# Performance work log

Hardware: AMD Instinct MI355X
Metric: run time of the kernel (lower is better)

## Reference

```python
import jax, jax.numpy as jnp
import numpy as np

HID = 512
HEADS = 8
HEAD_DIM = HID // HEADS
BS, SEQ = 4, 2048


def setup_inputs() -> dict:
    key = jax.random.key(0)
    ks = jax.random.split(key, 12)
    s = 0.02
    return {
        "query": jax.random.normal(ks[0], (BS, SEQ, HID), jnp.float32),
        "key": jax.random.normal(ks[1], (BS, SEQ, HID), jnp.float32),
        "value": jax.random.normal(ks[2], (BS, SEQ, HID), jnp.float32),
        "query_mask": jnp.ones((BS, SEQ), dtype=bool),
        "key_mask": jnp.ones((BS, SEQ), dtype=bool),
        "Wq": jax.random.normal(ks[3], (HID, HID), jnp.float32) * s,
        "bq": jnp.zeros((HID,), jnp.float32),
        "Wk": jax.random.normal(ks[4], (HID, HID), jnp.float32) * s,
        "bk": jnp.zeros((HID,), jnp.float32),
        "Wv": jax.random.normal(ks[5], (HID, HID), jnp.float32) * s,
        "bv": jnp.zeros((HID,), jnp.float32),
        "Wo": jax.random.normal(ks[6], (HID, HID), jnp.float32) * s,
        "bo": jnp.zeros((HID,), jnp.float32),
    }


def _mha(query, key, value, query_mask, key_mask, Wq, bq, Wk, bk, Wv, bv, Wo, bo):
    bs, q_len, _ = query.shape
    k_len = key.shape[1]
    scale = jnp.sqrt(jnp.asarray(HEAD_DIM, query.dtype))

    def proj(x, W, b):  # nn.Linear: x @ W^T + b, then split heads -> [b,h,s,d]
        y = jnp.einsum('bse,fe->bsf', x, W) + b
        return y.reshape(bs, -1, HEADS, HEAD_DIM).transpose(0, 2, 1, 3)

    q = proj(query, Wq, bq)
    k = proj(key, Wk, bk)
    v = proj(value, Wv, bv)

    energy = jnp.einsum('bhqd,bhkd->bhqk', q, k) / scale  # [b,h,q,k]
    neg = -jnp.finfo(energy.dtype).max

    pad_mask = query_mask[:, None, :, None] & key_mask[:, None, None, :]
    energy = jnp.where(pad_mask, energy, neg)

    # causal: mask positions where q_idx < k_idx
    causal = jnp.arange(q_len)[:, None] < jnp.arange(k_len)[None, :]
    energy = jnp.where(causal[None, None], neg, energy)

    attn = jax.nn.softmax(energy, axis=-1)  # dropout p=0.0 -> identity
    x = jnp.einsum('bhqk,bhkd->bhqd', attn, v)
    x = x.transpose(0, 2, 1, 3).reshape(bs, q_len, HID)
    return jnp.einsum('bse,fe->bsf', x, Wo) + bo


def reference(query, key, value, query_mask, key_mask, Wq, bq, Wk, bk, Wv, bv, Wo, bo):
    return _mha(query, key, value, query_mask, key_mask, Wq, bq, Wk, bk, Wv, bv, Wo, bo)
```

## Files before the change

### kernel.cpp

```cpp
#include <hip/hip_runtime.h>
#include <hip/hip_bf16.h>

#define DEVI __device__ __forceinline__

typedef __attribute__((ext_vector_type(4)))  float f32x4;
typedef __attribute__((ext_vector_type(16))) float f32x16;
typedef __attribute__((ext_vector_type(8)))  short bf16x8;

constexpr int BS    = 4;
constexpr int SEQ   = 2048;
constexpr int HID   = 512;
constexpr int HEADS = 8;
constexpr int HD    = 64;
constexpr int M     = BS * SEQ;

constexpr float QSCALE = 0.125f * 1.4426950408889634f;

DEVI ushort f2bf(float f) {
    union { float f; unsigned u; } a; a.f = f;
    unsigned r = a.u + 0x7fffu + ((a.u >> 16) & 1u);
    return (ushort)(r >> 16);
}

DEVI f32x4 mfma16(bf16x8 a, bf16x8 b, f32x4 c) {
    return __builtin_amdgcn_mfma_f32_16x16x32_bf16(a, b, c, 0, 0, 0);
}
DEVI f32x16 mfma32(bf16x8 a, bf16x8 b, f32x16 c) {
    return __builtin_amdgcn_mfma_f32_32x32x16_bf16(a, b, c, 0, 0, 0);
}

DEVI void gl_lds16(const ushort* g, ushort* l) {
    __builtin_amdgcn_global_load_lds(
        (const __attribute__((address_space(1))) void*)g,
        (__attribute__((address_space(3))) void*)l,
        16, 0, 0);
}

DEVI unsigned cvtpk(float lo, float hi) {
    unsigned r;
    asm("v_cvt_pk_bf16_f32 %0, %1, %2" : "=v"(r) : "v"(lo), "v"(hi));
    return r;
}

__global__ void cast_w(const float* __restrict__ wq, const float* __restrict__ wk,
                       const float* __restrict__ wv, const float* __restrict__ wo,
                       ushort* __restrict__ oq, ushort* __restrict__ ok,
                       ushort* __restrict__ ov, ushort* __restrict__ oo)
{
    const int NW4 = HID * HID / 4;
    int i = blockIdx.x * blockDim.x + threadIdx.x;
    const int a = i >> 16, j = i & (NW4 - 1);
    const float* src = (a == 0) ? wq : (a == 1) ? wk : (a == 2) ? wv : wo;
    ushort* dst = (a == 0) ? oq : (a == 1) ? ok : (a == 2) ? ov : oo;
    float4 f = ((const float4*)src)[j];
    ushort4 u;
    u.x = f2bf(f.x); u.y = f2bf(f.y); u.z = f2bf(f.z); u.w = f2bf(f.w);
    ((ushort4*)dst)[j] = u;
}

template<bool AF32>
DEVI void gemm_core(const void* __restrict__ Ain, const ushort* __restrict__ W,
                    const float* __restrict__ bias, void* __restrict__ out,
                    float scale, int mode, ushort* lA, ushort* lB)
{
    constexpr int BK = 32;
    const int tid  = threadIdx.x;
    const int lane = tid & 63, w = tid >> 6;
    const int wm = w >> 1, wn = w & 1;
    const int l15 = lane & 15, lg = lane >> 4;
    const int m0 = blockIdx.x * 128, n0 = blockIdx.y * 128;
    const int srow = tid >> 2, sc8 = (tid & 3) * 8;
    const int arow = tid >> 1, ach = (tid & 1) * 16;

    f32x4 acc[4][4];
    #pragma unroll
    for (int i = 0; i < 4; i++)
        #pragma unroll
        for (int n = 0; n < 4; n++) acc[i][n] = f32x4{0.f, 0.f, 0.f, 0.f};

    for (int k0 = 0; k0 < HID; k0 += BK) {
        if constexpr (AF32) {
            const float4* ap = (const float4*)((const float*)Ain +
                                (size_t)(m0 + arow) * HID + k0 + ach);
            const float4 a0 = ap[0], a1 = ap[1], a2 = ap[2], a3 = ap[3];
            union { unsigned u[4]; bf16x8 v; } p0, p1;
            p0.u[0] = cvtpk(a0.x, a0.y); p0.u[1] = cvtpk(a0.z, a0.w);
            p0.u[2] = cvtpk(a1.x, a1.y); p0.u[3] = cvtpk(a1.z, a1.w);
            p1.u[0] = cvtpk(a2.x, a2.y); p1.u[1] = cvtpk(a2.z, a2.w);
            p1.u[2] = cvtpk(a3.x, a3.y); p1.u[3] = cvtpk(a3.z, a3.w);
            *(bf16x8*)(lA + arow * 32 + ach)     = p0.v;
            *(bf16x8*)(lA + arow * 32 + ach + 8) = p1.v;
        } else {
            const ushort* A = (const ushort*)Ain;
            gl_lds16(A + (size_t)(m0 + srow) * HID + k0 + sc8, lA + w * 512);
            gl_lds16(A + (size_t)(m0 + 64 + srow) * HID + k0 + sc8, lA + 2048 + w * 512);
        }
        gl_lds16(W + (size_t)(n0 + srow) * HID + k0 + sc8, lB + w * 512);
        gl_lds16(W + (size_t)(n0 + 64 + srow) * HID + k0 + sc8, lB + 2048 + w * 512);
        __syncthreads();

        bf16x8 af[4], bfr[4];
        #pragma unroll
        for (int i = 0; i < 4; i++)
            af[i] = *(const bf16x8*)(lA + (wm * 64 + i * 16 + l15) * BK + lg * 8);
        #pragma unroll
        for (int n = 0; n < 4; n++)
            bfr[n] = *(const bf16x8*)(lB + (wn * 64 + n * 16 + l15) * BK + lg * 8);
        #pragma unroll
        for (int i = 0; i < 4; i++)
            #pragma unroll
            for (int n = 0; n < 4; n++)
                acc[i][n] = mfma16(af[i], bfr[n], acc[i][n]);
        __syncthreads();
    }

    #pragma unroll
    for (int i = 0; i < 4; i++) {
        #pragma unroll
        for (int n = 0; n < 4; n++) {
            const int col = n0 + wn * 64 + n * 16 + l15;
            const float bb = bias[col];
            const int rbase = m0 + wm * 64 + i * 16 + lg * 4;
            #pragma unroll
            for (int jj = 0; jj < 4; jj++) {
                float v = (acc[i][n][jj] + bb) * scale;
                const int r = rbase + jj;
                if (mode == 3) {
                    ((float*)out)[(size_t)r * HID + col] = v;
                } else {
                    const int b = r >> 11, s = r & (SEQ - 1);
                    const int h = col >> 6, d = col & 63;
                    const int bh = b * HEADS + h;
                    const int t = s >> 5;
                    const ushort u = f2bf(v);
                    if (mode == 0) {
                        const int l31r = s & 31;
                        const int ds = d >> 4, hif = (d >> 3) & 1, jf = d & 7;
                        ((ushort*)out)[(((size_t)bh * 64 + t) * 4 + ds) * 512 +
                                       (hif * 32 + l31r) * 8 + jf] = u;
                    } else {
                        const int c = s & 31;
                        const int kvh = (c >> 4) & 1, hif = (c >> 2) & 1;
                        const int jf = (c & 3) + ((c >> 3) & 1) * 4;
                        const int dt = d >> 5, drow = d & 31;
                        ((ushort*)out)[(((size_t)bh * 64 + t) * 4 + dt * 2 + kvh) * 512 +
                                       (hif * 32 + drow) * 8 + jf] = u;
                    }
                }
            }
        }
    }
}

__global__ __launch_bounds__(256)
void gemm_qkv(const float* __restrict__ Xq, const float* __restrict__ Xk,
              const float* __restrict__ Xv,
              const ushort* __restrict__ Wq, const ushort* __restrict__ Wk,
              const ushort* __restrict__ Wv,
              const float* __restrict__ bq, const float* __restrict__ bk,
              const float* __restrict__ bv,
              ushort* __restrict__ Qf, ushort* __restrict__ Kf,
              ushort* __restrict__ Vf)
{
    __shared__ ushort lA[128 * 32];
    __shared__ ushort lB[128 * 32];
    const int z = blockIdx.z;
    const float* A = z == 0 ? Xq : z == 1 ? Xk : Xv;
    const ushort* W = z == 0 ? Wq : z == 1 ? Wk : Wv;
    const float* bias = z == 0 ? bq : z == 1 ? bk : bv;
    void* out = z == 0 ? (void*)Qf : z == 1 ? (void*)Kf : (void*)Vf;
    gemm_core<true>(A, W, bias, out, z == 0 ? QSCALE : 1.0f, z == 2 ? 2 : 0, lA, lB);
}

__global__ __launch_bounds__(256)
void gemm_o(const ushort* __restrict__ ctx, const ushort* __restrict__ Wo,
            const float* __restrict__ bo, float* __restrict__ out)
{
    __shared__ ushort lA[128 * 32];
    __shared__ ushort lB[128 * 32];
    gemm_core<false>(ctx, Wo, bo, out, 1.0f, 3, lA, lB);
}

__global__ __launch_bounds__(256)
void attn5(const ushort* __restrict__ Qf, const ushort* __restrict__ Kf,
           const ushort* __restrict__ Vf, ushort* __restrict__ ctx)
{
    __shared__ float part[4][2][16][64];
    __shared__ float pml[4][2][32];

    const int tid  = threadIdx.x;
    const int lane = tid & 63, w = tid >> 6;
    const int l31 = lane & 31, hi = lane >> 5;

    const int bid = blockIdx.x;
    const int bh  = bid & 31;
    const int qt  = 63 - (bid >> 5);
    const int qb  = qt * 32;

    const ushort* Qb = Qf + ((size_t)bh * 64 + qt) * 2048;
    const ushort* Kb = Kf + (size_t)bh * 64 * 2048;
    const ushort* Vb = Vf + (size_t)bh * 64 * 2048;

    bf16x8 qf[4];
    #pragma unroll
    for (int ds = 0; ds < 4; ds++)
        qf[ds] = *(const bf16x8*)(Qb + ds * 512 + lane * 8);

    f32x16 acc0 = {}, acc1 = {};
    float mrun = -3e38f, lrun = 0.f;

    bf16x8 kf[4] = {}, va[4] = {};
    if (w <= qt) {
        const ushort* kp = Kb + (size_t)w * 2048 + lane * 8;
        const ushort* vp = Vb + (size_t)w * 2048 + lane * 8;
        #pragma unroll
        for (int ds = 0; ds < 4; ds++) {
            kf[ds] = *(const bf16x8*)(kp + ds * 512);
            va[ds] = *(const bf16x8*)(vp + ds * 512);
        }
    }

    for (int t = w; t <= qt; t += 4) {
        f32x16 s = {};
        #pragma unroll
        for (int ds = 0; ds < 4; ds++)
            s = mfma32(kf[ds], qf[ds], s);

        bf16x8 kfn[4], van[4];
        {
            const int tn = (t + 4 <= qt) ? t + 4 : t;
            const ushort* kp = Kb + (size_t)tn * 2048 + lane * 8;
            const ushort* vp = Vb + (size_t)tn * 2048 + lane * 8;
            #pragma unroll
            for (int ds = 0; ds < 4; ds++) {
                kfn[ds] = *(const bf16x8*)(kp + ds * 512);
                van[ds] = *(const bf16x8*)(vp + ds * 512);
            }
        }

        if (t == qt) {
            #pragma unroll
            for (int r = 0; r < 16; r++) {
                const int kvrow = (r & 3) + 8 * (r >> 2) + 4 * hi;
                s[r] = (kvrow > l31) ? -3e38f : s[r];
            }
        }

        float m8[8];
        #pragma unroll
        for (int r = 0; r < 8; r++) m8[r] = fmaxf(s[r], s[r + 8]);
        float m4a = fmaxf(m8[0], m8[1]), m4b = fmaxf(m8[2], m8[3]);
        float m4c = fmaxf(m8[4], m8[5]), m4d = fmaxf(m8[6], m8[7]);
        float pmax = fmaxf(fmaxf(m4a, m4b), fmaxf(m4c, m4d));
        pmax = fmaxf(pmax, __shfl_xor(pmax, 32));

        if (!__all(pmax <= mrun + 8.f)) {
            const float mnew = fmaxf(mrun, pmax);
            const float corr = __builtin_amdgcn_exp2f(mrun - mnew);
            lrun *= corr;
            #pragma unroll
            for (int r = 0; r < 16; r++) { acc0[r] *= corr; acc1[r] *= corr; }
            mrun = mnew;
        }

        float e[16];
        #pragma unroll
        for (int r = 0; r < 16; r++)
            e[r] = __builtin_amdgcn_exp2f(s[r] - mrun);
        float es0 = (e[0] + e[1]) + (e[2] + e[3]);
        float es1 = (e[4] + e[5]) + (e[6] + e[7]);
        float es2 = (e[8] + e[9]) + (e[10] + e[11]);
        float es3 = (e[12] + e[13]) + (e[14] + e[15]);
        float esum = (es0 + es1) + (es2 + es3);
        lrun += esum + __shfl_xor(esum, 32);

        union { unsigned u[4]; bf16x8 v; } pb0, pb1;
        pb0.u[0] = cvtpk(e[0],  e[1]);  pb0.u[1] = cvtpk(e[2],  e[3]);
        pb0.u[2] = cvtpk(e[4],  e[5]);  pb0.u[3] = cvtpk(e[6],  e[7]);
        pb1.u[0] = cvtpk(e[8],  e[9]);  pb1.u[1] = cvtpk(e[10], e[11]);
        pb1.u[2] = cvtpk(e[12], e[13]); pb1.u[3] = cvtpk(e[14], e[15]);

        acc0 = mfma32(va[0], pb0.v, acc0);
        acc0 = mfma32(va[1], pb1.v, acc0);
        acc1 = mfma32(va[2], pb0.v, acc1);
        acc1 = mfma32(va[3], pb1.v, acc1);

        #pragma unroll
        for (int ds = 0; ds < 4; ds++) { kf[ds] = kfn[ds]; va[ds] = van[ds]; }
    }

    #pragma unroll
    for (int r = 0; r < 16; r++) {
        part[w][0][r][lane] = acc0[r];
        part[w][1][r][lane] = acc1[r];
    }
    if (hi == 0) { pml[w][0][l31] = mrun; pml[w][1][l31] = lrun; }
    __syncthreads();

    const float mm0 = pml[0][0][l31], ll0 = pml[0][1][l31];
    const float mm1 = pml[1][0][l31], ll1 = pml[1][1][l31];
    const float mm2 = pml[2][0][l31], ll2 = pml[2][1][l31];
    const float mm3 = pml[3][0][l31], ll3 = pml[3][1][l31];
    const float mstar = fmaxf(fmaxf(mm0, mm1), fmaxf(mm2, mm3));
    const float f0 = __builtin_amdgcn_exp2f(mm0 - mstar);
    const float f1 = __builtin_amdgcn_exp2f(mm1 - mstar);
    const float f2 = __builtin_amdgcn_exp2f(mm2 - mstar);
    const float f3 = __builtin_amdgcn_exp2f(mm3 - mstar);
    const float lstar = ll0 * f0 + ll1 * f1 + ll2 * f2 + ll3 * f3;
    const float inv = 1.f / lstar;

    const int b = bh >> 3, h = bh & 7;
    ushort* op = ctx + ((size_t)(b * SEQ + qb + l31)) * HID + h * HD;
    #pragma unroll
    for (int a = 0; a < 2; a++) {
        float v[4];
        #pragma unroll
        for (int j = 0; j < 4; j++) {
            const int r = 4 * w + j;
            v[j] = (part[0][a][r][lane] * f0 + part[1][a][r][lane] * f1 +
                    part[2][a][r][lane] * f2 + part[3][a][r][lane] * f3) * inv;
        }
        ushort4 o;
        o.x = f2bf(v[0]); o.y = f2bf(v[1]); o.z = f2bf(v[2]); o.w = f2bf(v[3]);
        *(ushort4*)(op + a * 32 + 8 * w + 4 * hi) = o;
    }
}

extern "C" void kernel_launch(void* const* d_in, const int* in_sizes, int n_in,
                              void* d_out, int out_size, void* d_ws, size_t ws_size,
                              hipStream_t stream) {
    const float* q  = (const float*)d_in[0];
    const float* k  = (const float*)d_in[1];
    const float* v  = (const float*)d_in[2];
    const float* Wq = (const float*)d_in[5];
    const float* bq = (const float*)d_in[6];
    const float* Wk = (const float*)d_in[7];
    const float* bk = (const float*)d_in[8];
    const float* Wv = (const float*)d_in[9];
    const float* bv = (const float*)d_in[10];
    const float* Wo = (const float*)d_in[11];
    const float* bo = (const float*)d_in[12];

    char* ws = (char*)d_ws;
    constexpr size_t XSZ = (size_t)M * HID * 2;
    constexpr size_t WSZ = (size_t)HID * HID * 2;
    ushort* Wqb = (ushort*)(ws);
    ushort* Wkb = (ushort*)(ws + WSZ);
    ushort* Wvb = (ushort*)(ws + 2 * WSZ);
    ushort* Wob = (ushort*)(ws + 3 * WSZ);
    ushort* Qf  = (ushort*)(ws + 4 * WSZ);
    ushort* Kf  = (ushort*)(ws + 4 * WSZ + XSZ);
    ushort* Vf  = (ushort*)(ws + 4 * WSZ + 2 * XSZ);
    ushort* ctx = (ushort*)(ws + 4 * WSZ + 3 * XSZ);

    cast_w<<<1024, 256, 0, stream>>>(Wq, Wk, Wv, Wo, Wqb, Wkb, Wvb, Wob);

    dim3 gqkv(M / 128, HID / 128, 3);
    gemm_qkv<<<gqkv, 256, 0, stream>>>(q, k, v, Wqb, Wkb, Wvb,
                                       bq, bk, bv, Qf, Kf, Vf);

    attn5<<<BS * HEADS * (SEQ / 32), 256, 0, stream>>>(Qf, Kf, Vf, ctx);

    dim3 go(M / 128, HID / 128);
    gemm_o<<<go, 256, 0, stream>>>(ctx, Wob, bo, (float*)d_out);
}
```

Baseline: 92.95 us.

## Double-buffer GEMM LDS tiles and use 512-thread blocks with 8 warps

The projection GEMMs now double-buffer the A and B LDS tiles, prefetching the next K slice (global loads, plus fp32->bf16 conversion for the inputs) while the current slice feeds the MFMAs. This leaves one barrier per iteration instead of two. Blocks grow to 512 threads as a 2x4 warp grid, each warp computing 64x32 instead of 64x64. The aim is to hide global memory latency and raise occupancy, at the cost of double the LDS per block and more per-thread register pressure under launch_bounds(512,4).

```diff
diff --git a/kernel.cpp b/kernel.cpp
--- a/kernel.cpp
+++ b/kernel.cpp
@@ -63,62 +63,86 @@
                     const float* __restrict__ bias, void* __restrict__ out,
                     float scale, int mode, ushort* lA, ushort* lB)
 {
-    constexpr int BK = 32;
+    constexpr int BK = 32, NK = HID / BK;
     const int tid  = threadIdx.x;
     const int lane = tid & 63, w = tid >> 6;
-    const int wm = w >> 1, wn = w & 1;
+    const int wm = w >> 2, wn = w & 3;
     const int l15 = lane & 15, lg = lane >> 4;
     const int m0 = blockIdx.x * 128, n0 = blockIdx.y * 128;
     const int srow = tid >> 2, sc8 = (tid & 3) * 8;
-    const int arow = tid >> 1, ach = (tid & 1) * 16;
-
-    f32x4 acc[4][4];
+
+    f32x4 acc[4][2];
     #pragma unroll
     for (int i = 0; i < 4; i++)
         #pragma unroll
-        for (int n = 0; n < 4; n++) acc[i][n] = f32x4{0.f, 0.f, 0.f, 0.f};
-
-    for (int k0 = 0; k0 < HID; k0 += BK) {
-        if constexpr (AF32) {
-            const float4* ap = (const float4*)((const float*)Ain +
-                                (size_t)(m0 + arow) * HID + k0 + ach);
-            const float4 a0 = ap[0], a1 = ap[1], a2 = ap[2], a3 = ap[3];
-            union { unsigned u[4]; bf16x8 v; } p0, p1;
-            p0.u[0] = cvtpk(a0.x, a0.y); p0.u[1] = cvtpk(a0.z, a0.w);
-            p0.u[2] = cvtpk(a1.x, a1.y); p0.u[3] = cvtpk(a1.z, a1.w);
-            p1.u[0] = cvtpk(a2.x, a2.y); p1.u[1] = cvtpk(a2.z, a2.w);
-            p1.u[2] = cvtpk(a3.x, a3.y); p1.u[3] = cvtpk(a3.z, a3.w);
-            *(bf16x8*)(lA + arow * 32 + ach)     = p0.v;
-            *(bf16x8*)(lA + arow * 32 + ach + 8) = p1.v;
-        } else {
-            const ushort* A = (const ushort*)Ain;
-            gl_lds16(A + (size_t)(m0 + srow) * HID + k0 + sc8, lA + w * 512);
-            gl_lds16(A + (size_t)(m0 + 64 + srow) * HID + k0 + sc8, lA + 2048 + w * 512);
-        }
-        gl_lds16(W + (size_t)(n0 + srow) * HID + k0 + sc8, lB + w * 512);
-        gl_lds16(W + (size_t)(n0 + 64 + srow) * HID + k0 + sc8, lB + 2048 + w * 512);
+        for (int n = 0; n < 2; n++) acc[i][n] = f32x4{0.f, 0.f, 0.f, 0.f};
+
+    if constexpr (AF32) {
+        const float* A = (const float*)Ain;
+        const float4* ap = (const float4*)(A + (size_t)(m0 + srow) * HID + sc8);
+        const float4 a0 = ap[0], a1 = ap[1];
+        union { unsigned u[4]; bf16x8 v; } p;
+        p.u[0] = cvtpk(a0.x, a0.y); p.u[1] = cvtpk(a0.z, a0.w);
+        p.u[2] = cvtpk(a1.x, a1.y); p.u[3] = cvtpk(a1.z, a1.w);
+        *(bf16x8*)(lA + srow * 32 + sc8) = p.v;
+    } else {
+        gl_lds16((const ushort*)Ain + (size_t)(m0 + srow) * HID + sc8, lA + w * 512);
+    }
+    gl_lds16(W + (size_t)(n0 + srow) * HID + sc8, lB + w * 512);
+    __syncthreads();
+
+    int cur = 0;
+    for (int k = 0; k < NK; ++k) {
+        ushort* lAc = lA + cur * 4096;
+        ushort* lBc = lB + cur * 4096;
+        ushort* lAn = lA + (cur ^ 1) * 4096;
+        ushort* lBn = lB + (cur ^ 1) * 4096;
+        const int k1 = (k + 1) * BK;
+        const bool more = (k + 1 < NK);
+
+        float4 a0n, a1n;
+        if (more) {
+            if constexpr (AF32) {
+                const float* A = (const float*)Ain;
+                const float4* ap = (const float4*)(A + (size_t)(m0 + srow) * HID + k1 + sc8);
+                a0n = ap[0]; a1n = ap[1];
+            } else {
+                gl_lds16((const ushort*)Ain + (size_t)(m0 + srow) * HID + k1 + sc8,
+                         lAn + w * 512);
+            }
+            gl_lds16(W + (size_t)(n0 + srow) * HID + k1 + sc8, lBn + w * 512);
+        }
+
+        bf16x8 af[4], bfr[2];
+        #pragma unroll
+        for (int i = 0; i < 4; i++)
+            af[i] = *(const bf16x8*)(lAc + (wm * 64 + i * 16 + l15) * 32 + lg * 8);
+        #pragma unroll
+        for (int n = 0; n < 2; n++)
+            bfr[n] = *(const bf16x8*)(lBc + (wn * 32 + n * 16 + l15) * 32 + lg * 8);
+        #pragma unroll
+        for (int i = 0; i < 4; i++)
+            #pragma unroll
+            for (int n = 0; n < 2; n++)
+                acc[i][n] = mfma16(af[i], bfr[n], acc[i][n]);
+
+        if (more) {
+            if constexpr (AF32) {
+                union { unsigned u[4]; bf16x8 v; } p;
+                p.u[0] = cvtpk(a0n.x, a0n.y); p.u[1] = cvtpk(a0n.z, a0n.w);
+                p.u[2] = cvtpk(a1n.x, a1n.y); p.u[3] = cvtpk(a1n.z, a1n.w);
+                *(bf16x8*)(lAn + srow * 32 + sc8) = p.v;
+            }
+        }
         __syncthreads();
-
-        bf16x8 af[4], bfr[4];
-        #pragma unroll
-        for (int i = 0; i < 4; i++)
-            af[i] = *(const bf16x8*)(lA + (wm * 64 + i * 16 + l15) * BK + lg * 8);
-        #pragma unroll
-        for (int n = 0; n < 4; n++)
-            bfr[n] = *(const bf16x8*)(lB + (wn * 64 + n * 16 + l15) * BK + lg * 8);
-        #pragma unroll
-        for (int i = 0; i < 4; i++)
-            #pragma unroll
-            for (int n = 0; n < 4; n++)
-                acc[i][n] = mfma16(af[i], bfr[n], acc[i][n]);
-        __syncthreads();
+        cur ^= 1;
     }
 
     #pragma unroll
     for (int i = 0; i < 4; i++) {
         #pragma unroll
-        for (int n = 0; n < 4; n++) {
-            const int col = n0 + wn * 64 + n * 16 + l15;
+        for (int n = 0; n < 2; n++) {
+            const int col = n0 + wn * 32 + n * 16 + l15;
             const float bb = bias[col];
             const int rbase = m0 + wm * 64 + i * 16 + lg * 4;
             #pragma unroll
@@ -152,7 +176,7 @@
     }
 }
 
-__global__ __launch_bounds__(256)
+__global__ __launch_bounds__(512, 4)
 void gemm_qkv(const float* __restrict__ Xq, const float* __restrict__ Xk,
               const float* __restrict__ Xv,
               const ushort* __restrict__ Wq, const ushort* __restrict__ Wk,
@@ -162,8 +186,8 @@
               ushort* __restrict__ Qf, ushort* __restrict__ Kf,
               ushort* __restrict__ Vf)
 {
-    __shared__ ushort lA[128 * 32];
-    __shared__ ushort lB[128 * 32];
+    __shared__ ushort lA[2 * 128 * 32];
+    __shared__ ushort lB[2 * 128 * 32];
     const int z = blockIdx.z;
     const float* A = z == 0 ? Xq : z == 1 ? Xk : Xv;
     const ushort* W = z == 0 ? Wq : z == 1 ? Wk : Wv;
@@ -172,12 +196,12 @@
     gemm_core<true>(A, W, bias, out, z == 0 ? QSCALE : 1.0f, z == 2 ? 2 : 0, lA, lB);
 }
 
-__global__ __launch_bounds__(256)
+__global__ __launch_bounds__(512, 4)
 void gemm_o(const ushort* __restrict__ ctx, const ushort* __restrict__ Wo,
             const float* __restrict__ bo, float* __restrict__ out)
 {
-    __shared__ ushort lA[128 * 32];
-    __shared__ ushort lB[128 * 32];
+    __shared__ ushort lA[2 * 128 * 32];
+    __shared__ ushort lB[2 * 128 * 32];
     gemm_core<false>(ctx, Wo, bo, out, 1.0f, 3, lA, lB);
 }
 
@@ -356,11 +380,11 @@
     cast_w<<<1024, 256, 0, stream>>>(Wq, Wk, Wv, Wo, Wqb, Wkb, Wvb, Wob);
 
     dim3 gqkv(M / 128, HID / 128, 3);
-    gemm_qkv<<<gqkv, 256, 0, stream>>>(q, k, v, Wqb, Wkb, Wvb,
+    gemm_qkv<<<gqkv, 512, 0, stream>>>(q, k, v, Wqb, Wkb, Wvb,
                                        bq, bk, bv, Qf, Kf, Vf);
 
     attn5<<<BS * HEADS * (SEQ / 32), 256, 0, stream>>>(Qf, Kf, Vf, ctx);
 
     dim3 go(M / 128, HID / 128);
-    gemm_o<<<go, 256, 0, stream>>>(ctx, Wob, bo, (float*)d_out);
-}
+    gemm_o<<<go, 512, 0, stream>>>(ctx, Wob, bo, (float*)d_out);
+}
```

Result: no change. 91.62 us (-1.4%).
